# Kernel optimization log

Hardware: AMD Instinct MI355X
Metric: run time of the kernel (lower is better)

## Reference

```python
import jax, jax.numpy as jnp
import numpy as np

TAU = 0.7
N_NODES = 1024
N_EDGES = 32768

def _mlp3(x, W1, b1, W2, b2, W3, b3):
    h = jax.nn.relu(x @ W1 + b1)
    h = jax.nn.relu(h @ W2 + b2)
    return h @ W3 + b3

def _gcn_conv(x, src, dst, W, b, n):
    # PyG GCNConv(add_self_loops=False): out = D^-1/2 A D^-1/2 (x W) + b
    deg = jax.ops.segment_sum(jnp.ones(src.shape[0], x.dtype), dst, num_segments=n)
    dinv = jnp.where(deg > 0, jax.lax.rsqrt(jnp.maximum(deg, 1.0)), 0.0)
    h = x @ W
    msg = h[src] * (dinv[src] * dinv[dst])[:, None]
    return jax.ops.segment_sum(msg, dst, num_segments=n) + b

def _forward(x1, x11, x2, mlp_W1, mlp_b1, mlp_W2, mlp_b2, mlp_W3, mlp_b3,
             m1_W1, m1_b1, m1_W2, m1_b2, m1_W3, m1_b3,
             wm1, bp1, bp2, wm12, wm13, class2,
             gcn1_W, gcn1_b, wm2, gcn2_W, gcn2_b, fc_W, fc_b, src, dst):
    n = x1.shape[0]
    logits = _mlp3(x1, mlp_W1, mlp_b1, mlp_W2, mlp_b2, mlp_W3, mlp_b3)  # [N,3]
    g = _mlp3(x11, m1_W1, m1_b1, m1_W2, m1_b2, m1_W3, m1_b3)            # [N,2]
    # hard argmax routing, softened: tau at argmax, (1-tau)/2 at the 2 others
    oh = jax.nn.one_hot(jnp.argmax(logits, axis=1), 3, dtype=logits.dtype)
    r = oh * TAU + (1.0 - oh) * ((1.0 - TAU) * 0.5)                     # [N,3]
    # fused form of: (einsum('nj,jkl',g,class2) * x2[...,None]).sum(-1) + g@b1
    res1 = jnp.einsum('nj,jkl,nk->nk', g, class2, x2) + g @ bp1         # [N,768]
    # fused form of: (einsum('nj,jkl',r,wm1) * res1[...,None]).sum(-1) + r@b2
    res1 = jnp.einsum('nj,jkl,nk->nk', r, wm1, res1) + r @ bp2          # [N,768]
    h1 = jax.nn.relu(_gcn_conv(res1, src, dst, gcn1_W, gcn1_b, n))      # [N,256]
    h1 = (r @ wm12) * h1 + 2e-4 * (res1 @ wm13)                         # [N,256]
    res2 = jnp.einsum('nj,jkl,nk->nk', r, wm2, h1)                      # [N,256]
    h2 = jax.nn.relu(_gcn_conv(res2, src, dst, gcn2_W, gcn2_b, n))      # [N,32]
    return jax.nn.log_softmax(h2 @ fc_W + fc_b, axis=1)                 # [N,8]

def setup_inputs():
    key = jax.random.key(0)
    ks = jax.random.split(key, 32)
    f = jnp.float32
    nrm = lambda i, s, sc=0.05: sc * jax.random.normal(ks[i], s, f)
    return {
        'x1': nrm(0, (N_NODES, 768), 1.0),
        'x11': nrm(1, (N_NODES, 768), 1.0),
        'x2': nrm(2, (N_NODES, 768), 1.0),
        'mlp_W1': nrm(3, (768, 512)), 'mlp_b1': jnp.zeros((512,), f),
        'mlp_W2': nrm(4, (512, 512)), 'mlp_b2': jnp.zeros((512,), f),
        'mlp_W3': nrm(5, (512, 3)), 'mlp_b3': jnp.zeros((3,), f),
        'm1_W1': nrm(6, (768, 512)), 'm1_b1': jnp.zeros((512,), f),
        'm1_W2': nrm(7, (512, 512)), 'm1_b2': jnp.zeros((512,), f),
        'm1_W3': nrm(8, (512, 2)), 'm1_b3': jnp.zeros((2,), f),
        'wm1': nrm(9, (3, 768, 256)),
        'bp1': jnp.zeros((2, 768), f),
        'bp2': jnp.zeros((3, 768), f),
        'wm12': jnp.ones((3, 256), f),
        'wm13': nrm(10, (768, 256)),
        'class2': jnp.ones((2, 768, 64), f),
        'gcn1_W': nrm(11, (768, 256)), 'gcn1_b': jnp.zeros((256,), f),
        'wm2': nrm(12, (3, 256, 256)),
        'gcn2_W': nrm(13, (256, 32)), 'gcn2_b': jnp.zeros((32,), f),
        'fc_W': nrm(14, (32, 8)), 'fc_b': jnp.zeros((8,), f),
        'edge_index': jax.random.randint(ks[15], (2, N_EDGES), 0, N_NODES),
    }

def reference(x1, x11, x2, mlp_W1, mlp_b1, mlp_W2, mlp_b2, mlp_W3, mlp_b3,
              m1_W1, m1_b1, m1_W2, m1_b2, m1_W3, m1_b3,
              wm1, bp1, bp2, wm12, wm13, class2,
              gcn1_W, gcn1_b, wm2, gcn2_W, gcn2_b, fc_W, fc_b, edge_index):
    src, dst = edge_index[0], edge_index[1]
    return _forward(x1, x11, x2, mlp_W1, mlp_b1, mlp_W2, mlp_b2, mlp_W3, mlp_b3,
                    m1_W1, m1_b1, m1_W2, m1_b2, m1_W3, m1_b3,
                    wm1, bp1, bp2, wm12, wm13, class2,
                    gcn1_W, gcn1_b, wm2, gcn2_W, gcn2_b, fc_W, fc_b, src, dst)
```

## Files before the change

kernel.cpp:

```cpp
#include <hip/hip_runtime.h>
#include <hip/hip_bf16.h>

#define NN 1024
#define NE 32768
#define TAU 0.7f
#define GAPT 0.01f

typedef __attribute__((ext_vector_type(8))) short short8;
typedef __attribute__((ext_vector_type(4))) float f32x4;

__device__ inline ushort bf16rne(float x) {
    union { float f; unsigned u; } a; a.f = x;
    unsigned r = (a.u + 0x7FFFu + ((a.u >> 16) & 1u)) >> 16;
    return (ushort)r;
}
__device__ inline float bf16tof(ushort h) {
    union { unsigned u; float f; } a; a.u = ((unsigned)h) << 16;
    return a.f;
}
__device__ inline void bf16split(float x, ushort& h, ushort& l) {
    h = bf16rne(x);
    l = bf16rne(x - bf16tof(h));
}

template <int K, int EPI>
__device__ __forceinline__ void gemm_wave(
    int lane, int rt, int ct,
    const ushort* __restrict__ Ah, const ushort* __restrict__ Al,
    const ushort* __restrict__ Bh, const ushort* __restrict__ Bl,
    const float* __restrict__ bias, const float* __restrict__ W3,
    float* __restrict__ Cf, ushort* __restrict__ Oh, ushort* __restrict__ Ol, int N) {
    int r0 = rt * 16, c0 = ct * 32;
    int g = lane >> 4, q = lane & 15;
    const ushort* pah = Ah + (size_t)(r0 + q) * K + g * 8;
    const ushort* pal = Al + (size_t)(r0 + q) * K + g * 8;
    const ushort* pb0h = Bh + (size_t)(c0 + q) * K + g * 8;
    const ushort* pb0l = Bl + (size_t)(c0 + q) * K + g * 8;
    const ushort* pb1h = pb0h + (size_t)16 * K;
    const ushort* pb1l = pb0l + (size_t)16 * K;
    f32x4 acc0 = {0.f, 0.f, 0.f, 0.f};
    f32x4 acc1 = {0.f, 0.f, 0.f, 0.f};
#pragma unroll 2
    for (int k0 = 0; k0 < K; k0 += 32) {
        short8 ah = *(const short8*)(pah + k0);
        short8 al = *(const short8*)(pal + k0);
        short8 b0h = *(const short8*)(pb0h + k0);
        short8 b0l = *(const short8*)(pb0l + k0);
        short8 b1h = *(const short8*)(pb1h + k0);
        short8 b1l = *(const short8*)(pb1l + k0);
        acc0 = __builtin_amdgcn_mfma_f32_16x16x32_bf16(ah, b0h, acc0, 0, 0, 0);
        acc1 = __builtin_amdgcn_mfma_f32_16x16x32_bf16(ah, b1h, acc1, 0, 0, 0);
        acc0 = __builtin_amdgcn_mfma_f32_16x16x32_bf16(ah, b0l, acc0, 0, 0, 0);
        acc1 = __builtin_amdgcn_mfma_f32_16x16x32_bf16(ah, b1l, acc1, 0, 0, 0);
        acc0 = __builtin_amdgcn_mfma_f32_16x16x32_bf16(al, b0h, acc0, 0, 0, 0);
        acc1 = __builtin_amdgcn_mfma_f32_16x16x32_bf16(al, b1h, acc1, 0, 0, 0);
    }
    int col0 = c0 + q, col1 = c0 + 16 + q;
    if constexpr (EPI == 0) {
#pragma unroll
        for (int i = 0; i < 4; i++) {
            int row = r0 + g * 4 + i;
            Cf[(size_t)row * N + col0] = acc0[i];
            Cf[(size_t)row * N + col1] = acc1[i];
        }
    } else if constexpr (EPI == 1) {
        float bv0 = bias[col0], bv1 = bias[col1];
#pragma unroll
        for (int i = 0; i < 4; i++) {
            int row = r0 + g * 4 + i;
            float a0 = fmaxf(acc0[i] + bv0, 0.f);
            float a1 = fmaxf(acc1[i] + bv1, 0.f);
            ushort h, l;
            bf16split(a0, h, l);
            Oh[(size_t)row * N + col0] = h;
            Ol[(size_t)row * N + col0] = l;
            bf16split(a1, h, l);
            Oh[(size_t)row * N + col1] = h;
            Ol[(size_t)row * N + col1] = l;
        }
    } else {
        constexpr int J = (EPI == 2) ? 3 : 2;
        constexpr int STR = (EPI == 2) ? 4 : 2;
        float bv0 = bias[col0], bv1 = bias[col1];
        float s[4][J];
#pragma unroll
        for (int i = 0; i < 4; i++) {
            float a0 = fmaxf(acc0[i] + bv0, 0.f);
            float a1 = fmaxf(acc1[i] + bv1, 0.f);
#pragma unroll
            for (int j = 0; j < J; j++)
                s[i][j] = a0 * W3[col0 * J + j] + a1 * W3[col1 * J + j];
        }
#pragma unroll
        for (int i = 0; i < 4; i++)
#pragma unroll
            for (int j = 0; j < J; j++) {
                float v = s[i][j];
#pragma unroll
                for (int m = 1; m < 16; m <<= 1) v += __shfl_xor(v, m);
                s[i][j] = v;
            }
        if (q == 0) {
#pragma unroll
            for (int i = 0; i < 4; i++) {
                int row = r0 + g * 4 + i;
#pragma unroll
                for (int j = 0; j < J; j++) atomicAdd(&Cf[(size_t)row * STR + j], s[i][j]);
            }
        }
    }
}

template <int M, int N, int K, int EPI>
__global__ __launch_bounds__(256) void gemm3(
    const ushort* __restrict__ Ah, const ushort* __restrict__ Al,
    const ushort* __restrict__ Bh, const ushort* __restrict__ Bl,
    float* __restrict__ Cf) {
    constexpr int RT = M / 16;
    constexpr int JOBS = RT * (N / 32);
    int wid = (blockIdx.x * 256 + threadIdx.x) >> 6;
    if (wid >= JOBS) return;
    gemm_wave<K, EPI>(threadIdx.x & 63, wid % RT, wid / RT, Ah, Al, Bh, Bl,
                      nullptr, nullptr, Cf, nullptr, nullptr, N);
}

template <int K, int EPI0, int EPI1, int RIDER>
__global__ __launch_bounds__(256) void gemm_pair(
    const ushort* __restrict__ Ah0, const ushort* __restrict__ Al0,
    const ushort* __restrict__ Bh0, const ushort* __restrict__ Bl0,
    const float* __restrict__ bias0, const float* __restrict__ W30,
    float* __restrict__ Cf0, ushort* __restrict__ Oh0, ushort* __restrict__ Ol0,
    const ushort* __restrict__ Ah1, const ushort* __restrict__ Al1,
    const ushort* __restrict__ Bh1, const ushort* __restrict__ Bl1,
    const float* __restrict__ bias1, const float* __restrict__ W31,
    float* __restrict__ Cf1, ushort* __restrict__ Oh1, ushort* __restrict__ Ol1,
    const int* __restrict__ esrc, const int* __restrict__ edst,
    const int* __restrict__ deg, int* __restrict__ rowst, int* __restrict__ cursor,
    float* __restrict__ dinv, int* __restrict__ adj) {
    if (RIDER == 1 && blockIdx.x >= 512) {
        __shared__ int ps[256];
        int t = threadIdx.x;
        int4 d4 = *(const int4*)(deg + t * 4);
        int sum = d4.x + d4.y + d4.z + d4.w;
        ps[t] = sum;
        __syncthreads();
        for (int off = 1; off < 256; off <<= 1) {
            int v = (t >= off) ? ps[t - off] : 0;
            __syncthreads();
            ps[t] += v;
            __syncthreads();
        }
        int r0 = ps[t] - sum;
        int r1 = r0 + d4.x, r2 = r1 + d4.y, r3 = r2 + d4.z;
        rowst[t * 4 + 0] = r0;
        rowst[t * 4 + 1] = r1;
        rowst[t * 4 + 2] = r2;
        rowst[t * 4 + 3] = r3;
        if (t == 255) rowst[1024] = r3 + d4.w;
        cursor[t * 4 + 0] = r0;
        cursor[t * 4 + 1] = r1;
        cursor[t * 4 + 2] = r2;
        cursor[t * 4 + 3] = r3;
        dinv[t * 4 + 0] = d4.x > 0 ? rsqrtf((float)d4.x) : 0.f;
        dinv[t * 4 + 1] = d4.y > 0 ? rsqrtf((float)d4.y) : 0.f;
        dinv[t * 4 + 2] = d4.z > 0 ? rsqrtf((float)d4.z) : 0.f;
        dinv[t * 4 + 3] = d4.w > 0 ? rsqrtf((float)d4.w) : 0.f;
        return;
    }
    if (RIDER == 2 && blockIdx.x >= 512) {
        int e = (blockIdx.x - 512) * 256 + threadIdx.x;
        int d = edst[e];
        int slot = atomicAdd(&cursor[d], 1);
        adj[slot] = esrc[e];
        return;
    }
    int wid = (blockIdx.x * 256 + threadIdx.x) >> 6;
    int lane = threadIdx.x & 63;
    int pair = wid >> 10;
    int widl = wid & 1023;
    int rt = widl & 63, ct = widl >> 6;
    if (pair == 0)
        gemm_wave<K, EPI0>(lane, rt, ct, Ah0, Al0, Bh0, Bl0, bias0, W30, Cf0, Oh0, Ol0, 512);
    else
        gemm_wave<K, EPI1>(lane, rt, ct, Ah1, Al1, Bh1, Bl1, bias1, W31, Cf1, Oh1, Ol1, 512);
}

__device__ void dev_zero(int sub, int t, float* zbase) {
    for (int i = sub * 256 + t; i < 6144; i += 512) zbase[i] = 0.f;
}

__device__ void dev_tabs_wave(int gw, int lane, const float* __restrict__ class2,
                              const float* __restrict__ wm1, const float* __restrict__ wm2,
                              float* __restrict__ C2s, float* __restrict__ Wm1s,
                              float* __restrict__ Wm2s) {
    if (gw < 2304) {
        float4 v = *(const float4*)(wm1 + (size_t)gw * 256 + lane * 4);
        float s = v.x + v.y + v.z + v.w;
#pragma unroll
        for (int m = 32; m; m >>= 1) s += __shfl_xor(s, m);
        if (lane == 0) Wm1s[gw] = s;
    } else if (gw < 3072) {
        int j = gw - 2304;
        float4 v = *(const float4*)(wm2 + (size_t)j * 256 + lane * 4);
        float s = v.x + v.y + v.z + v.w;
#pragma unroll
        for (int m = 32; m; m >>= 1) s += __shfl_xor(s, m);
        if (lane == 0) Wm2s[j] = s;
    } else {
        int row = (gw - 3072) * 4 + (lane >> 4);
        float4 v = *(const float4*)(class2 + (size_t)row * 64 + (lane & 15) * 4);
        float s = v.x + v.y + v.z + v.w;
#pragma unroll
        for (int m = 8; m; m >>= 1) s += __shfl_xor(s, m);
        if ((lane & 15) == 0) C2s[row] = s;
    }
}

__device__ void dev_splitx(int sub, int t, const float* __restrict__ X,
                           ushort* __restrict__ Xh, ushort* __restrict__ Xl) {
    int j = sub * 256 + t;
    float4 v = ((const float4*)X)[j];
    ushort h0, l0, h1, l1, h2, l2, h3, l3;
    bf16split(v.x, h0, l0);
    bf16split(v.y, h1, l1);
    bf16split(v.z, h2, l2);
    bf16split(v.w, h3, l3);
    ((ushort4*)Xh)[j] = make_ushort4(h0, h1, h2, h3);
    ((ushort4*)Xl)[j] = make_ushort4(l0, l1, l2, l3);
}

__global__ __launch_bounds__(1024) void aux0(
    const float* class2, const float* wm1, const float* wm2,
    float* C2s, float* Wm1s, float* Wm2s, float* zbase,
    const float* x1, ushort* XH1, ushort* XL1,
    const float* x11, ushort* XH2, ushort* XL2,
    const float* W1a, ushort* W1AH, ushort* W1AL,
    const float* W1b, ushort* W1BH, ushort* W1BL,
    const float* W2a, ushort* W2AH, ushort* W2AL,
    const float* W2b, ushort* W2BH, ushort* W2BL,
    const float* G1W, ushort* GWH, ushort* GWL,
    const float* W13, const float* G2W, ushort* G2TH, ushort* G2TL,
    const int* edst, int* deg) {
    __shared__ float tb[4][32][33];
    int quad = threadIdx.x >> 8;
    int t = threadIdx.x & 255;
    int sub = blockIdx.x * 4 + quad;
    if (sub >= 4202) return;
    const float* W = nullptr;
    ushort *Th = nullptr, *Tl = nullptr;
    int K = 0, N = 0, tile = 0;
    if (sub >= 4074) {
        int e = (sub - 4074) * 256 + t;
        atomicAdd(&deg[edst[e]], 1);
    }
    else if (sub >= 4066) { W = G2W; Th = G2TH; Tl = G2TL; K = 256; N = 32;  tile = sub - 4066; }
    else if (sub >= 3874) { W = W13; Th = GWH + 256 * 768; Tl = GWL + 256 * 768; K = 768; N = 256; tile = sub - 3874; }
    else if (sub >= 3682) { W = G1W; Th = GWH; Tl = GWL; K = 768; N = 256; tile = sub - 3682; }
    else if (sub >= 3426) { W = W2b; Th = W2BH; Tl = W2BL; K = 512; N = 512; tile = sub - 3426; }
    else if (sub >= 3170) { W = W2a; Th = W2AH; Tl = W2AL; K = 512; N = 512; tile = sub - 3170; }
    else if (sub >= 2786) { W = W1b; Th = W1BH; Tl = W1BL; K = 768; N = 512; tile = sub - 2786; }
    else if (sub >= 2402) { W = W1a; Th = W1AH; Tl = W1AL; K = 768; N = 512; tile = sub - 2402; }
    int k0 = 0, n0 = 0;
    if (W) {
        k0 = (tile % (K / 32)) * 32;
        n0 = (tile / (K / 32)) * 32;
        int tx = t % 32, ty = t / 32;
        for (int i = ty; i < 32; i += 8)
            tb[quad][i][tx] = W[(size_t)(k0 + i) * N + n0 + tx];
    } else if (sub < 2) dev_zero(sub, t, zbase);
    else if (sub < 866) dev_tabs_wave((sub - 2) * 4 + (t >> 6), t & 63,
                                      class2, wm1, wm2, C2s, Wm1s, Wm2s);
    else if (sub < 1634) dev_splitx(sub - 866, t, x1, XH1, XL1);
    else if (sub < 2402) dev_splitx(sub - 1634, t, x11, XH2, XL2);
    __syncthreads();
    if (W) {
        int tx = t % 32, ty = t / 32;
        for (int i = ty; i < 32; i += 8) {
            float v = tb[quad][tx][i];
            ushort h, l;
            bf16split(v, h, l);
            Th[(size_t)(n0 + i) * K + k0 + tx] = h;
            Tl[(size_t)(n0 + i) * K + k0 + tx] = l;
        }
    }
}

__global__ __launch_bounds__(256) void finrep(
    const float* __restrict__ LG, const float* __restrict__ b3, float* __restrict__ rbuf,
    const float* __restrict__ x1, const float* __restrict__ W1, const float* __restrict__ b1,
    const float* __restrict__ W2, const float* __restrict__ b2, const float* __restrict__ W3) {
    __shared__ int snode[4];
    __shared__ int scnt;
    __shared__ float part[4][512];
    __shared__ float xs[768];
    __shared__ float h1[512];
    __shared__ float h2[512];
    int t = threadIdx.x;
    if (t == 0) scnt = 0;
    __syncthreads();
    if (t < 4) {
        int n = blockIdx.x * 4 + t;
        float l0 = LG[n * 4 + 0] + b3[0];
        float l1 = LG[n * 4 + 1] + b3[1];
        float l2 = LG[n * 4 + 2] + b3[2];
        int am = 0;
        float mv = l0;
        if (l1 > mv) { mv = l1; am = 1; }
        if (l2 > mv) { mv = l2; am = 2; }
        float sec = (am == 0) ? fmaxf(l1, l2) : ((am == 1) ? fmaxf(l0, l2) : fmaxf(l0, l1));
        float lo = (1.f - TAU) * 0.5f;
        rbuf[n * 4 + 0] = (am == 0) ? TAU : lo;
        rbuf[n * 4 + 1] = (am == 1) ? TAU : lo;
        rbuf[n * 4 + 2] = (am == 2) ? TAU : lo;
        if (mv - sec < GAPT) {
            int s = atomicAdd(&scnt, 1);
            snode[s] = n;
        }
    }
    __syncthreads();
    int cnt = scnt;
    int w = t >> 6, l = t & 63;
    for (int it = 0; it < cnt; it++) {
        int n = snode[it];
        for (int k = t; k < 768; k += 256) xs[k] = x1[(size_t)n * 768 + k];
        __syncthreads();
        {
            float acc[8] = {0.f, 0.f, 0.f, 0.f, 0.f, 0.f, 0.f, 0.f};
            for (int k = w * 192; k < (w + 1) * 192; k++) {
                float xv = xs[k];
                const float* wr = W1 + (size_t)k * 512 + l;
#pragma unroll
                for (int c = 0; c < 8; c++) acc[c] += xv * wr[64 * c];
            }
#pragma unroll
            for (int c = 0; c < 8; c++) part[w][l + 64 * c] = acc[c];
        }
        __syncthreads();
        for (int d = t; d < 512; d += 256)
            h1[d] = fmaxf(part[0][d] + part[1][d] + part[2][d] + part[3][d] + b1[d], 0.f);
        __syncthreads();
        {
            float acc[8] = {0.f, 0.f, 0.f, 0.f, 0.f, 0.f, 0.f, 0.f};
            for (int k = w * 128; k < (w + 1) * 128; k++) {
                float xv = h1[k];
                const float* wr = W2 + (size_t)k * 512 + l;
#pragma unroll
                for (int c = 0; c < 8; c++) acc[c] += xv * wr[64 * c];
            }
#pragma unroll
            for (int c = 0; c < 8; c++) part[w][l + 64 * c] = acc[c];
        }
        __syncthreads();
        for (int d = t; d < 512; d += 256)
            h2[d] = fmaxf(part[0][d] + part[1][d] + part[2][d] + part[3][d] + b2[d], 0.f);
        __syncthreads();
        if (t < 64) {
            float p0 = 0.f, p1 = 0.f, p2 = 0.f;
            for (int k = t; k < 512; k += 64) {
                float hv = h2[k];
                p0 += hv * W3[k * 3 + 0];
                p1 += hv * W3[k * 3 + 1];
                p2 += hv * W3[k * 3 + 2];
            }
            for (int off = 32; off; off >>= 1) {
                p0 += __shfl_down(p0, off);
                p1 += __shfl_down(p1, off);
                p2 += __shfl_down(p2, off);
            }
            if (t == 0) {
                float l0 = p0 + b3[0], l1 = p1 + b3[1], l2 = p2 + b3[2];
                int am = 0;
                float mv = l0;
                if (l1 > mv) { mv = l1; am = 1; }
                if (l2 > mv) { mv = l2; am = 2; }
                float lo = (1.f - TAU) * 0.5f;
                rbuf[n * 4 + 0] = (am == 0) ? TAU : lo;
                rbuf[n * 4 + 1] = (am == 1) ? TAU : lo;
                rbuf[n * 4 + 2] = (am == 2) ? TAU : lo;
            }
        }
        __syncthreads();
    }
}

__global__ __launch_bounds__(256) void res1_kernel(
    const float* __restrict__ x2, const float* __restrict__ G, const float* __restrict__ m1b3,
    const float* __restrict__ rbuf, const float* __restrict__ C2s, const float* __restrict__ bp1,
    const float* __restrict__ Wm1s, const float* __restrict__ bp2,
    ushort* __restrict__ r1h, ushort* __restrict__ r1l) {
    int idx = blockIdx.x * 256 + threadIdx.x;
    int n = idx / 192;
    int kq = (idx % 192) * 4;
    float g0 = G[n * 2 + 0] + m1b3[0], g1 = G[n * 2 + 1] + m1b3[1];
    float r0 = rbuf[n * 4 + 0], r1 = rbuf[n * 4 + 1], r2 = rbuf[n * 4 + 2];
    float4 xv = *(const float4*)(x2 + (size_t)n * 768 + kq);
    float4 c0 = *(const float4*)(C2s + kq);
    float4 c1 = *(const float4*)(C2s + 768 + kq);
    float4 p0 = *(const float4*)(bp1 + kq);
    float4 p1 = *(const float4*)(bp1 + 768 + kq);
    float4 w0 = *(const float4*)(Wm1s + kq);
    float4 w1 = *(const float4*)(Wm1s + 768 + kq);
    float4 w2 = *(const float4*)(Wm1s + 1536 + kq);
    float4 q0 = *(const float4*)(bp2 + kq);
    float4 q1 = *(const float4*)(bp2 + 768 + kq);
    float4 q2 = *(const float4*)(bp2 + 1536 + kq);
    float o[4];
    o[0] = (xv.x * (g0 * c0.x + g1 * c1.x) + g0 * p0.x + g1 * p1.x) * (r0 * w0.x + r1 * w1.x + r2 * w2.x) + r0 * q0.x + r1 * q1.x + r2 * q2.x;
    o[1] = (xv.y * (g0 * c0.y + g1 * c1.y) + g0 * p0.y + g1 * p1.y) * (r0 * w0.y + r1 * w1.y + r2 * w2.y) + r0 * q0.y + r1 * q1.y + r2 * q2.y;
    o[2] = (xv.z * (g0 * c0.z + g1 * c1.z) + g0 * p0.z + g1 * p1.z) * (r0 * w0.z + r1 * w1.z + r2 * w2.z) + r0 * q0.z + r1 * q1.z + r2 * q2.z;
    o[3] = (xv.w * (g0 * c0.w + g1 * c1.w) + g0 * p0.w + g1 * p1.w) * (r0 * w0.w + r1 * w1.w + r2 * w2.w) + r0 * q0.w + r1 * q1.w + r2 * q2.w;
    ushort h[4], l[4];
#pragma unroll
    for (int i = 0; i < 4; i++) bf16split(o[i], h[i], l[i]);
    size_t off = ((size_t)n * 768 + kq) / 4;
    ((ushort4*)r1h)[off] = make_ushort4(h[0], h[1], h[2], h[3]);
    ((ushort4*)r1l)[off] = make_ushort4(l[0], l[1], l[2], l[3]);
}

__global__ __launch_bounds__(256) void gather1_combine(
    const float* __restrict__ gcw, const int* __restrict__ rowst, const int* __restrict__ adj,
    const float* __restrict__ dinv, const float* __restrict__ gcn1_b,
    const float* __restrict__ rbuf, const float* __restrict__ wm12,
    const float* __restrict__ Wm2s, ushort* __restrict__ res2h, ushort* __restrict__ res2l) {
    int n = blockIdx.x;
    int k = threadIdx.x;
    int lane = threadIdx.x & 63;
    int e0 = rowst[n], e1 = rowst[n + 1];
    float acc = 0.f;
    for (int base = e0; base < e1; base += 64) {
        int idx = base + lane;
        int s_i = 0;
        float w_i = 0.f;
        if (idx < e1) { s_i = adj[idx]; w_i = dinv[s_i]; }
        int mm = min(64, e1 - base);
        for (int j = 0; j < mm; j++) {
            int s = __shfl(s_i, j);
            float w = __shfl(w_i, j);
            acc += gcw[(size_t)s * 512 + k] * w;
        }
    }
    float h1 = dinv[n] * acc + gcn1_b[k];
    float mv = gcw[(size_t)n * 512 + 256 + k];
    float r0 = rbuf[n * 4 + 0], r1 = rbuf[n * 4 + 1], r2 = rbuf[n * 4 + 2];
    float a = r0 * wm12[k] + r1 * wm12[256 + k] + r2 * wm12[512 + k];
    float w = r0 * Wm2s[k] + r1 * Wm2s[256 + k] + r2 * Wm2s[512 + k];
    float v = w * (a * fmaxf(h1, 0.f) + 2e-4f * mv);
    ushort h, l;
    bf16split(v, h, l);
    res2h[(size_t)n * 256 + k] = h;
    res2l[(size_t)n * 256 + k] = l;
}

__global__ __launch_bounds__(64) void gather2_fc(
    const float* __restrict__ g2h, const int* __restrict__ rowst, const int* __restrict__ adj,
    const float* __restrict__ dinv, const float* __restrict__ gcn2_b,
    const float* __restrict__ fcW, const float* __restrict__ fcb, float* __restrict__ out) {
    __shared__ float h2s[2][32];
    int t = threadIdx.x;
    int half = t >> 5, k = t & 31;
    int n = blockIdx.x * 2 + half;
    int e0 = rowst[n], e1 = rowst[n + 1];
    float acc = 0.f;
    for (int base = e0; base < e1; base += 32) {
        int idx = base + k;
        int s_i = 0;
        float w_i = 0.f;
        if (idx < e1) { s_i = adj[idx]; w_i = dinv[s_i]; }
        int mm = min(32, e1 - base);
        for (int j = 0; j < mm; j++) {
            int s = __shfl(s_i, j, 32);
            float w = __shfl(w_i, j, 32);
            acc += g2h[(size_t)s * 32 + k] * w;
        }
    }
    h2s[half][k] = fmaxf(dinv[n] * acc + gcn2_b[k], 0.f);
    __syncthreads();
    if (t < 16) {
        int nn = t >> 3, j = t & 7;
        const float* hr = h2s[nn];
        float logit = fcb[j];
#pragma unroll
        for (int i = 0; i < 32; i++) logit += hr[i] * fcW[i * 8 + j];
        float m = logit;
        for (int off = 4; off; off >>= 1) m = fmaxf(m, __shfl_xor(m, off, 8));
        float e = expf(logit - m), s = e;
        for (int off = 4; off; off >>= 1) s += __shfl_xor(s, off, 8);
        out[(size_t)(blockIdx.x * 2 + nn) * 8 + j] = logit - m - logf(s);
    }
}

extern "C" void kernel_launch(void* const* d_in, const int* in_sizes, int n_in,
                              void* d_out, int out_size, void* d_ws, size_t ws_size,
                              hipStream_t stream) {
    const float* x1     = (const float*)d_in[0];
    const float* x11    = (const float*)d_in[1];
    const float* x2     = (const float*)d_in[2];
    const float* mlp_W1 = (const float*)d_in[3];
    const float* mlp_b1 = (const float*)d_in[4];
    const float* mlp_W2 = (const float*)d_in[5];
    const float* mlp_b2 = (const float*)d_in[6];
    const float* mlp_W3 = (const float*)d_in[7];
    const float* mlp_b3 = (const float*)d_in[8];
    const float* m1_W1  = (const float*)d_in[9];
    const float* m1_b1  = (const float*)d_in[10];
    const float* m1_W2  = (const float*)d_in[11];
    const float* m1_b2  = (const float*)d_in[12];
    const float* m1_W3  = (const float*)d_in[13];
    const float* m1_b3  = (const float*)d_in[14];
    const float* wm1    = (const float*)d_in[15];
    const float* bp1    = (const float*)d_in[16];
    const float* bp2    = (const float*)d_in[17];
    const float* wm12   = (const float*)d_in[18];
    const float* wm13   = (const float*)d_in[19];
    const float* class2 = (const float*)d_in[20];
    const float* gcn1_W = (const float*)d_in[21];
    const float* gcn1_b = (const float*)d_in[22];
    const float* wm2    = (const float*)d_in[23];
    const float* gcn2_W = (const float*)d_in[24];
    const float* gcn2_b = (const float*)d_in[25];
    const float* fc_W   = (const float*)d_in[26];
    const float* fc_b   = (const float*)d_in[27];
    const int* eidx     = (const int*)d_in[28];
    const int* esrc = eidx;
    const int* edst = eidx + NE;

    char* ws = (char*)d_ws;
    ushort* XH1   = (ushort*)(ws + 0x0000000);
    ushort* XL1   = (ushort*)(ws + 0x0180000);
    ushort* XH2   = (ushort*)(ws + 0x0300000);
    ushort* XL2   = (ushort*)(ws + 0x0480000);
    ushort* W1AH  = (ushort*)(ws + 0x0600000);
    ushort* W1AL  = (ushort*)(ws + 0x06C0000);
    ushort* W1BH  = (ushort*)(ws + 0x0780000);
    ushort* W1BL  = (ushort*)(ws + 0x0840000);
    ushort* W2AH  = (ushort*)(ws + 0x0900000);
    ushort* W2AL  = (ushort*)(ws + 0x0980000);
    ushort* W2BH  = (ushort*)(ws + 0x0A00000);
    ushort* W2BL  = (ushort*)(ws + 0x0A80000);
    ushort* GWH   = (ushort*)(ws + 0x0B00000);
    ushort* GWL   = (ushort*)(ws + 0x0BC0000);
    ushort* G2TH  = (ushort*)(ws + 0x0C80000);
    ushort* G2TL  = (ushort*)(ws + 0x0C84000);
    ushort* HS1AH = (ushort*)(ws + 0x0D00000);
    ushort* HS1AL = (ushort*)(ws + 0x0E00000);
    ushort* HS1BH = (ushort*)(ws + 0x0F00000);
    ushort* HS1BL = (ushort*)(ws + 0x1000000);
    ushort* RES1H = (ushort*)(ws + 0x1100000);
    ushort* RES1L = (ushort*)(ws + 0x1280000);
    float*  GCW   = (float*)(ws + 0x1400000);
    ushort* RES2H = (ushort*)(ws + 0x1600000);
    ushort* RES2L = (ushort*)(ws + 0x1680000);
    float*  G2H   = (float*)(ws + 0x1700000);
    float* LOGITS = (float*)(ws + 0x1740000);
    float* GBUF   = (float*)(ws + 0x1744000);
    float* RBUF   = (float*)(ws + 0x1746000);
    float* DINV   = (float*)(ws + 0x174A000);
    int*   ROWST  = (int*)(ws + 0x174B000);
    int*   CURS   = (int*)(ws + 0x174D000);
    int*   ADJ    = (int*)(ws + 0x174E000);
    int*   DEG    = (int*)(ws + 0x176E000);
    float* C2S    = (float*)(ws + 0x1770000);
    float* WM1S   = (float*)(ws + 0x1772000);
    float* WM2S   = (float*)(ws + 0x1775000);

    hipMemsetAsync(DEG, 0, NN * sizeof(int), stream);
    aux0<<<1051, 1024, 0, stream>>>(class2, wm1, wm2, C2S, WM1S, WM2S, LOGITS,
                                    x1, XH1, XL1, x11, XH2, XL2,
                                    mlp_W1, W1AH, W1AL, m1_W1, W1BH, W1BL,
                                    mlp_W2, W2AH, W2AL, m1_W2, W2BH, W2BL,
                                    gcn1_W, GWH, GWL, wm13, gcn2_W, G2TH, G2TL,
                                    edst, DEG);
    gemm_pair<768, 1, 1, 1><<<513, 256, 0, stream>>>(
        XH1, XL1, W1AH, W1AL, mlp_b1, nullptr, nullptr, HS1AH, HS1AL,
        XH2, XL2, W1BH, W1BL, m1_b1, nullptr, nullptr, HS1BH, HS1BL,
        esrc, edst, DEG, ROWST, CURS, DINV, ADJ);
    gemm_pair<512, 2, 3, 2><<<640, 256, 0, stream>>>(
        HS1AH, HS1AL, W2AH, W2AL, mlp_b2, mlp_W3, LOGITS, nullptr, nullptr,
        HS1BH, HS1BL, W2BH, W2BL, m1_b2, m1_W3, GBUF, nullptr, nullptr,
        esrc, edst, DEG, ROWST, CURS, DINV, ADJ);
    finrep<<<256, 256, 0, stream>>>(LOGITS, mlp_b3, RBUF, x1, mlp_W1, mlp_b1,
                                    mlp_W2, mlp_b2, mlp_W3);
    res1_kernel<<<768, 256, 0, stream>>>(x2, GBUF, m1_b3, RBUF, C2S, bp1, WM1S, bp2,
                                         RES1H, RES1L);
    gemm3<1024, 512, 768, 0><<<256, 256, 0, stream>>>(RES1H, RES1L, GWH, GWL, GCW);
    gather1_combine<<<NN, 256, 0, stream>>>(GCW, ROWST, ADJ, DINV, gcn1_b, RBUF,
                                            wm12, WM2S, RES2H, RES2L);
    gemm3<1024, 32, 256, 0><<<16, 256, 0, stream>>>(RES2H, RES2L, G2TH, G2TL, G2H);
    gather2_fc<<<NN / 2, 64, 0, stream>>>(G2H, ROWST, ADJ, DINV, gcn2_b, fc_W, fc_b,
                                          (float*)d_out);
}
```

Before: 177.2 us.

## Fuse routing finalize into res1, and fold GCN2 GEMM into aggregation

Merges the routing-finalization kernel with the res1 elementwise kernel, so r values come from shared memory and one launch is removed. The second GCN layer is reordered: neighbours are aggregated over the 256-wide res2 first and then multiplied by gcn2_W inside the gather kernel, which drops the separate split-bf16 GEMM, the gcn2_W transpose work in aux0 and the res2 bf16 split. The cost is that the gather now reads 256 floats per edge instead of 32, so gather traffic grows eightfold, and the fused res1 runs on 256 blocks instead of 768.

```diff
diff --git a/kernel.cpp b/kernel.cpp
--- a/kernel.cpp
+++ b/kernel.cpp
@@ -239,21 +239,19 @@
     const float* W2a, ushort* W2AH, ushort* W2AL,
     const float* W2b, ushort* W2BH, ushort* W2BL,
     const float* G1W, ushort* GWH, ushort* GWL,
-    const float* W13, const float* G2W, ushort* G2TH, ushort* G2TL,
-    const int* edst, int* deg) {
+    const float* W13, const int* edst, int* deg) {
     __shared__ float tb[4][32][33];
     int quad = threadIdx.x >> 8;
     int t = threadIdx.x & 255;
     int sub = blockIdx.x * 4 + quad;
-    if (sub >= 4202) return;
+    if (sub >= 4194) return;
     const float* W = nullptr;
     ushort *Th = nullptr, *Tl = nullptr;
     int K = 0, N = 0, tile = 0;
-    if (sub >= 4074) {
-        int e = (sub - 4074) * 256 + t;
+    if (sub >= 4066) {
+        int e = (sub - 4066) * 256 + t;
         atomicAdd(&deg[edst[e]], 1);
     }
-    else if (sub >= 4066) { W = G2W; Th = G2TH; Tl = G2TL; K = 256; N = 32;  tile = sub - 4066; }
     else if (sub >= 3874) { W = W13; Th = GWH + 256 * 768; Tl = GWL + 256 * 768; K = 768; N = 256; tile = sub - 3874; }
     else if (sub >= 3682) { W = G1W; Th = GWH; Tl = GWL; K = 768; N = 256; tile = sub - 3682; }
     else if (sub >= 3426) { W = W2b; Th = W2BH; Tl = W2BL; K = 512; N = 512; tile = sub - 3426; }
@@ -285,12 +283,17 @@
     }
 }
 
-__global__ __launch_bounds__(256) void finrep(
+__global__ __launch_bounds__(256) void finrep_res1(
     const float* __restrict__ LG, const float* __restrict__ b3, float* __restrict__ rbuf,
     const float* __restrict__ x1, const float* __restrict__ W1, const float* __restrict__ b1,
-    const float* __restrict__ W2, const float* __restrict__ b2, const float* __restrict__ W3) {
+    const float* __restrict__ W2, const float* __restrict__ b2, const float* __restrict__ W3,
+    const float* __restrict__ x2, const float* __restrict__ G, const float* __restrict__ m1b3,
+    const float* __restrict__ C2s, const float* __restrict__ bp1,
+    const float* __restrict__ Wm1s, const float* __restrict__ bp2,
+    ushort* __restrict__ r1h, ushort* __restrict__ r1l) {
     __shared__ int snode[4];
     __shared__ int scnt;
+    __shared__ float rloc[4][3];
     __shared__ float part[4][512];
     __shared__ float xs[768];
     __shared__ float h1[512];
@@ -309,9 +312,11 @@
         if (l2 > mv) { mv = l2; am = 2; }
         float sec = (am == 0) ? fmaxf(l1, l2) : ((am == 1) ? fmaxf(l0, l2) : fmaxf(l0, l1));
         float lo = (1.f - TAU) * 0.5f;
-        rbuf[n * 4 + 0] = (am == 0) ? TAU : lo;
-        rbuf[n * 4 + 1] = (am == 1) ? TAU : lo;
-        rbuf[n * 4 + 2] = (am == 2) ? TAU : lo;
+        float v0 = (am == 0) ? TAU : lo;
+        float v1 = (am == 1) ? TAU : lo;
+        float v2 = (am == 2) ? TAU : lo;
+        rbuf[n * 4 + 0] = v0; rbuf[n * 4 + 1] = v1; rbuf[n * 4 + 2] = v2;
+        rloc[t][0] = v0; rloc[t][1] = v1; rloc[t][2] = v2;
         if (mv - sec < GAPT) {
             int s = atomicAdd(&scnt, 1);
             snode[s] = n;
@@ -374,54 +379,53 @@
                 if (l1 > mv) { mv = l1; am = 1; }
                 if (l2 > mv) { mv = l2; am = 2; }
                 float lo = (1.f - TAU) * 0.5f;
-                rbuf[n * 4 + 0] = (am == 0) ? TAU : lo;
-                rbuf[n * 4 + 1] = (am == 1) ? TAU : lo;
-                rbuf[n * 4 + 2] = (am == 2) ? TAU : lo;
+                float v0 = (am == 0) ? TAU : lo;
+                float v1 = (am == 1) ? TAU : lo;
+                float v2 = (am == 2) ? TAU : lo;
+                rbuf[n * 4 + 0] = v0; rbuf[n * 4 + 1] = v1; rbuf[n * 4 + 2] = v2;
+                int ln = n & 3;
+                rloc[ln][0] = v0; rloc[ln][1] = v1; rloc[ln][2] = v2;
             }
         }
         __syncthreads();
     }
-}
-
-__global__ __launch_bounds__(256) void res1_kernel(
-    const float* __restrict__ x2, const float* __restrict__ G, const float* __restrict__ m1b3,
-    const float* __restrict__ rbuf, const float* __restrict__ C2s, const float* __restrict__ bp1,
-    const float* __restrict__ Wm1s, const float* __restrict__ bp2,
-    ushort* __restrict__ r1h, ushort* __restrict__ r1l) {
-    int idx = blockIdx.x * 256 + threadIdx.x;
-    int n = idx / 192;
-    int kq = (idx % 192) * 4;
-    float g0 = G[n * 2 + 0] + m1b3[0], g1 = G[n * 2 + 1] + m1b3[1];
-    float r0 = rbuf[n * 4 + 0], r1 = rbuf[n * 4 + 1], r2 = rbuf[n * 4 + 2];
-    float4 xv = *(const float4*)(x2 + (size_t)n * 768 + kq);
-    float4 c0 = *(const float4*)(C2s + kq);
-    float4 c1 = *(const float4*)(C2s + 768 + kq);
-    float4 p0 = *(const float4*)(bp1 + kq);
-    float4 p1 = *(const float4*)(bp1 + 768 + kq);
-    float4 w0 = *(const float4*)(Wm1s + kq);
-    float4 w1 = *(const float4*)(Wm1s + 768 + kq);
-    float4 w2 = *(const float4*)(Wm1s + 1536 + kq);
-    float4 q0 = *(const float4*)(bp2 + kq);
-    float4 q1 = *(const float4*)(bp2 + 768 + kq);
-    float4 q2 = *(const float4*)(bp2 + 1536 + kq);
-    float o[4];
-    o[0] = (xv.x * (g0 * c0.x + g1 * c1.x) + g0 * p0.x + g1 * p1.x) * (r0 * w0.x + r1 * w1.x + r2 * w2.x) + r0 * q0.x + r1 * q1.x + r2 * q2.x;
-    o[1] = (xv.y * (g0 * c0.y + g1 * c1.y) + g0 * p0.y + g1 * p1.y) * (r0 * w0.y + r1 * w1.y + r2 * w2.y) + r0 * q0.y + r1 * q1.y + r2 * q2.y;
-    o[2] = (xv.z * (g0 * c0.z + g1 * c1.z) + g0 * p0.z + g1 * p1.z) * (r0 * w0.z + r1 * w1.z + r2 * w2.z) + r0 * q0.z + r1 * q1.z + r2 * q2.z;
-    o[3] = (xv.w * (g0 * c0.w + g1 * c1.w) + g0 * p0.w + g1 * p1.w) * (r0 * w0.w + r1 * w1.w + r2 * w2.w) + r0 * q0.w + r1 * q1.w + r2 * q2.w;
-    ushort h[4], l[4];
-#pragma unroll
-    for (int i = 0; i < 4; i++) bf16split(o[i], h[i], l[i]);
-    size_t off = ((size_t)n * 768 + kq) / 4;
-    ((ushort4*)r1h)[off] = make_ushort4(h[0], h[1], h[2], h[3]);
-    ((ushort4*)r1l)[off] = make_ushort4(l[0], l[1], l[2], l[3]);
+    float gm0 = m1b3[0], gm1 = m1b3[1];
+    for (int qd = t; qd < 768; qd += 256) {
+        int ln = qd / 192;
+        int kq = (qd % 192) * 4;
+        int n = blockIdx.x * 4 + ln;
+        float g0 = G[n * 2 + 0] + gm0, g1 = G[n * 2 + 1] + gm1;
+        float r0 = rloc[ln][0], r1 = rloc[ln][1], r2 = rloc[ln][2];
+        float4 xv = *(const float4*)(x2 + (size_t)n * 768 + kq);
+        float4 c0 = *(const float4*)(C2s + kq);
+        float4 c1 = *(const float4*)(C2s + 768 + kq);
+        float4 p0 = *(const float4*)(bp1 + kq);
+        float4 p1 = *(const float4*)(bp1 + 768 + kq);
+        float4 w0 = *(const float4*)(Wm1s + kq);
+        float4 w1 = *(const float4*)(Wm1s + 768 + kq);
+        float4 w2 = *(const float4*)(Wm1s + 1536 + kq);
+        float4 q0 = *(const float4*)(bp2 + kq);
+        float4 q1 = *(const float4*)(bp2 + 768 + kq);
+        float4 q2 = *(const float4*)(bp2 + 1536 + kq);
+        float o[4];
+        o[0] = (xv.x * (g0 * c0.x + g1 * c1.x) + g0 * p0.x + g1 * p1.x) * (r0 * w0.x + r1 * w1.x + r2 * w2.x) + r0 * q0.x + r1 * q1.x + r2 * q2.x;
+        o[1] = (xv.y * (g0 * c0.y + g1 * c1.y) + g0 * p0.y + g1 * p1.y) * (r0 * w0.y + r1 * w1.y + r2 * w2.y) + r0 * q0.y + r1 * q1.y + r2 * q2.y;
+        o[2] = (xv.z * (g0 * c0.z + g1 * c1.z) + g0 * p0.z + g1 * p1.z) * (r0 * w0.z + r1 * w1.z + r2 * w2.z) + r0 * q0.z + r1 * q1.z + r2 * q2.z;
+        o[3] = (xv.w * (g0 * c0.w + g1 * c1.w) + g0 * p0.w + g1 * p1.w) * (r0 * w0.w + r1 * w1.w + r2 * w2.w) + r0 * q0.w + r1 * q1.w + r2 * q2.w;
+        ushort hh[4], ll[4];
+#pragma unroll
+        for (int i = 0; i < 4; i++) bf16split(o[i], hh[i], ll[i]);
+        size_t off = ((size_t)n * 768 + kq) / 4;
+        ((ushort4*)r1h)[off] = make_ushort4(hh[0], hh[1], hh[2], hh[3]);
+        ((ushort4*)r1l)[off] = make_ushort4(ll[0], ll[1], ll[2], ll[3]);
+    }
 }
 
 __global__ __launch_bounds__(256) void gather1_combine(
     const float* __restrict__ gcw, const int* __restrict__ rowst, const int* __restrict__ adj,
     const float* __restrict__ dinv, const float* __restrict__ gcn1_b,
     const float* __restrict__ rbuf, const float* __restrict__ wm12,
-    const float* __restrict__ Wm2s, ushort* __restrict__ res2h, ushort* __restrict__ res2l) {
+    const float* __restrict__ Wm2s, float* __restrict__ res2f) {
     int n = blockIdx.x;
     int k = threadIdx.x;
     int lane = threadIdx.x & 63;
@@ -444,48 +448,60 @@
     float r0 = rbuf[n * 4 + 0], r1 = rbuf[n * 4 + 1], r2 = rbuf[n * 4 + 2];
     float a = r0 * wm12[k] + r1 * wm12[256 + k] + r2 * wm12[512 + k];
     float w = r0 * Wm2s[k] + r1 * Wm2s[256 + k] + r2 * Wm2s[512 + k];
-    float v = w * (a * fmaxf(h1, 0.f) + 2e-4f * mv);
-    ushort h, l;
-    bf16split(v, h, l);
-    res2h[(size_t)n * 256 + k] = h;
-    res2l[(size_t)n * 256 + k] = l;
-}
-
-__global__ __launch_bounds__(64) void gather2_fc(
-    const float* __restrict__ g2h, const int* __restrict__ rowst, const int* __restrict__ adj,
-    const float* __restrict__ dinv, const float* __restrict__ gcn2_b,
-    const float* __restrict__ fcW, const float* __restrict__ fcb, float* __restrict__ out) {
-    __shared__ float h2s[2][32];
+    res2f[(size_t)n * 256 + k] = w * (a * fmaxf(h1, 0.f) + 2e-4f * mv);
+}
+
+__global__ __launch_bounds__(256) void gather2_full(
+    const float* __restrict__ res2f, const int* __restrict__ rowst,
+    const int* __restrict__ adj, const float* __restrict__ dinv,
+    const float* __restrict__ G2W, const float* __restrict__ gcn2_b,
+    const float* __restrict__ fcW, const float* __restrict__ fcb,
+    float* __restrict__ out) {
+    __shared__ float gres[256];
+    __shared__ float part[8][32];
     int t = threadIdx.x;
-    int half = t >> 5, k = t & 31;
-    int n = blockIdx.x * 2 + half;
+    int lane = t & 63;
+    int n = blockIdx.x;
     int e0 = rowst[n], e1 = rowst[n + 1];
     float acc = 0.f;
-    for (int base = e0; base < e1; base += 32) {
-        int idx = base + k;
+    for (int base = e0; base < e1; base += 64) {
+        int idx = base + lane;
         int s_i = 0;
         float w_i = 0.f;
         if (idx < e1) { s_i = adj[idx]; w_i = dinv[s_i]; }
-        int mm = min(32, e1 - base);
+        int mm = min(64, e1 - base);
         for (int j = 0; j < mm; j++) {
-            int s = __shfl(s_i, j, 32);
-            float w = __shfl(w_i, j, 32);
-            acc += g2h[(size_t)s * 32 + k] * w;
-        }
-    }
-    h2s[half][k] = fmaxf(dinv[n] * acc + gcn2_b[k], 0.f);
+            int s = __shfl(s_i, j);
+            float w = __shfl(w_i, j);
+            acc += res2f[(size_t)s * 256 + t] * w;
+        }
+    }
+    gres[t] = acc * dinv[n];
     __syncthreads();
-    if (t < 16) {
-        int nn = t >> 3, j = t & 7;
-        const float* hr = h2s[nn];
-        float logit = fcb[j];
-#pragma unroll
-        for (int i = 0; i < 32; i++) logit += hr[i] * fcW[i * 8 + j];
+    int j = t & 31, seg = t >> 5;
+    float p = 0.f;
+#pragma unroll
+    for (int kk = 0; kk < 32; kk++) {
+        int k = seg * 32 + kk;
+        p += gres[k] * G2W[k * 32 + j];
+    }
+    part[seg][j] = p;
+    __syncthreads();
+    if (t < 32) {
+        float h2 = part[0][t] + part[1][t] + part[2][t] + part[3][t] +
+                   part[4][t] + part[5][t] + part[6][t] + part[7][t] + gcn2_b[t];
+        gres[t] = fmaxf(h2, 0.f);
+    }
+    __syncthreads();
+    if (t < 8) {
+        float logit = fcb[t];
+#pragma unroll
+        for (int i = 0; i < 32; i++) logit += gres[i] * fcW[i * 8 + t];
         float m = logit;
         for (int off = 4; off; off >>= 1) m = fmaxf(m, __shfl_xor(m, off, 8));
         float e = expf(logit - m), s = e;
         for (int off = 4; off; off >>= 1) s += __shfl_xor(s, off, 8);
-        out[(size_t)(blockIdx.x * 2 + nn) * 8 + j] = logit - m - logf(s);
+        out[(size_t)n * 8 + t] = logit - m - logf(s);
     }
 }
 
@@ -539,8 +555,6 @@
     ushort* W2BL  = (ushort*)(ws + 0x0A80000);
     ushort* GWH   = (ushort*)(ws + 0x0B00000);
     ushort* GWL   = (ushort*)(ws + 0x0BC0000);
-    ushort* G2TH  = (ushort*)(ws + 0x0C80000);
-    ushort* G2TL  = (ushort*)(ws + 0x0C84000);
     ushort* HS1AH = (ushort*)(ws + 0x0D00000);
     ushort* HS1AL = (ushort*)(ws + 0x0E00000);
     ushort* HS1BH = (ushort*)(ws + 0x0F00000);
@@ -548,9 +562,7 @@
     ushort* RES1H = (ushort*)(ws + 0x1100000);
     ushort* RES1L = (ushort*)(ws + 0x1280000);
     float*  GCW   = (float*)(ws + 0x1400000);
-    ushort* RES2H = (ushort*)(ws + 0x1600000);
-    ushort* RES2L = (ushort*)(ws + 0x1680000);
-    float*  G2H   = (float*)(ws + 0x1700000);
+    float*  RES2F = (float*)(ws + 0x1600000);
     float* LOGITS = (float*)(ws + 0x1740000);
     float* GBUF   = (float*)(ws + 0x1744000);
     float* RBUF   = (float*)(ws + 0x1746000);
@@ -564,12 +576,11 @@
     float* WM2S   = (float*)(ws + 0x1775000);
 
     hipMemsetAsync(DEG, 0, NN * sizeof(int), stream);
-    aux0<<<1051, 1024, 0, stream>>>(class2, wm1, wm2, C2S, WM1S, WM2S, LOGITS,
+    aux0<<<1049, 1024, 0, stream>>>(class2, wm1, wm2, C2S, WM1S, WM2S, LOGITS,
                                     x1, XH1, XL1, x11, XH2, XL2,
                                     mlp_W1, W1AH, W1AL, m1_W1, W1BH, W1BL,
                                     mlp_W2, W2AH, W2AL, m1_W2, W2BH, W2BL,
-                                    gcn1_W, GWH, GWL, wm13, gcn2_W, G2TH, G2TL,
-                                    edst, DEG);
+                                    gcn1_W, GWH, GWL, wm13, edst, DEG);
     gemm_pair<768, 1, 1, 1><<<513, 256, 0, stream>>>(
         XH1, XL1, W1AH, W1AL, mlp_b1, nullptr, nullptr, HS1AH, HS1AL,
         XH2, XL2, W1BH, W1BL, m1_b1, nullptr, nullptr, HS1BH, HS1BL,
@@ -578,14 +589,13 @@
         HS1AH, HS1AL, W2AH, W2AL, mlp_b2, mlp_W3, LOGITS, nullptr, nullptr,
         HS1BH, HS1BL, W2BH, W2BL, m1_b2, m1_W3, GBUF, nullptr, nullptr,
         esrc, edst, DEG, ROWST, CURS, DINV, ADJ);
-    finrep<<<256, 256, 0, stream>>>(LOGITS, mlp_b3, RBUF, x1, mlp_W1, mlp_b1,
-                                    mlp_W2, mlp_b2, mlp_W3);
-    res1_kernel<<<768, 256, 0, stream>>>(x2, GBUF, m1_b3, RBUF, C2S, bp1, WM1S, bp2,
+    finrep_res1<<<256, 256, 0, stream>>>(LOGITS, mlp_b3, RBUF, x1, mlp_W1, mlp_b1,
+                                         mlp_W2, mlp_b2, mlp_W3,
+                                         x2, GBUF, m1_b3, C2S, bp1, WM1S, bp2,
                                          RES1H, RES1L);
     gemm3<1024, 512, 768, 0><<<256, 256, 0, stream>>>(RES1H, RES1L, GWH, GWL, GCW);
     gather1_combine<<<NN, 256, 0, stream>>>(GCW, ROWST, ADJ, DINV, gcn1_b, RBUF,
-                                            wm12, WM2S, RES2H, RES2L);
-    gemm3<1024, 32, 256, 0><<<16, 256, 0, stream>>>(RES2H, RES2L, G2TH, G2TL, G2H);
-    gather2_fc<<<NN / 2, 64, 0, stream>>>(G2H, ROWST, ADJ, DINV, gcn2_b, fc_W, fc_b,
-                                          (float*)d_out);
-}
+                                            wm12, WM2S, RES2F);
+    gather2_full<<<NN, 256, 0, stream>>>(RES2F, ROWST, ADJ, DINV, gcn2_W, gcn2_b,
+                                         fc_W, fc_b, (float*)d_out);
+}
```

Measured after the change: 343.8 us. 94.0% more time.
